# Optimization experiments

Measured on AMD Instinct MI355X. Metric: run time of the kernel, lower is better.

Reference implementation:

```python
import jax, jax.numpy as jnp
import numpy as np

B, C, H, W = 8, 256, 64, 64
CK = 64  # C // k with k=4


def setup_inputs() -> dict:
    key = jax.random.key(0)
    ks = jax.random.split(key, 5)
    s = 1.0 / np.sqrt(C)
    return {
        "x": jax.random.normal(ks[0], (B, C, H, W), dtype=jnp.float32),
        "wq": jax.random.normal(ks[1], (CK, C), dtype=jnp.float32) * s,
        "bq": jnp.zeros((CK,), dtype=jnp.float32),
        "wk": jax.random.normal(ks[2], (CK, C), dtype=jnp.float32) * s,
        "bk": jnp.zeros((CK,), dtype=jnp.float32),
        "wv": jax.random.normal(ks[3], (C, C), dtype=jnp.float32) * s,
        "bv": jnp.zeros((C,), dtype=jnp.float32),
        "wg": jax.random.normal(ks[4], (C, C), dtype=jnp.float32) * s,
        "bg": jnp.zeros((C,), dtype=jnp.float32),
    }


def reference(x, wq, bq, wk, bk, wv, bv, wg, bg):
    b, c, h, w = x.shape
    n = h * w
    xf = x.reshape(b, c, n)  # [B, C, N]
    # 1x1 convs are channel-wise matmuls
    q = jnp.einsum('oc,bcn->bon', wq, xf) + bq[None, :, None]  # [B, Ck, N]
    k = jnp.einsum('oc,bcn->bon', wk, xf) + bk[None, :, None]  # [B, Ck, N]
    v = jnp.einsum('oc,bcn->bon', wv, xf) + bv[None, :, None]  # [B, C, N]
    # energy[b,i,j] = q[b,:,i] . k[b,:,j]
    energy = jnp.einsum('bci,bcj->bij', q, k)  # [B, N, N]
    energy = jax.nn.elu(energy) / n
    out = jnp.einsum('bcn,bnj->bcj', v, energy).reshape(b, c, h, w)
    out = jnp.einsum('oc,bchw->bohw', wg, out) + bg[None, :, None, None]
    return out
```

## Files before the change

### kernel.cpp

```cpp
#include <hip/hip_runtime.h>
#include <math.h>

#define BATCH 8
#define CH    256
#define NPIX  4096
#define CKDIM 64

typedef __attribute__((ext_vector_type(8))) short short8;
typedef __attribute__((ext_vector_type(4))) float f32x4;

#define MFMA16x16(a, b, c) __builtin_amdgcn_mfma_f32_16x16x32_bf16((a), (b), (c), 0, 0, 0)

__device__ __forceinline__ unsigned short f2bf(float f) {
    union { float f; unsigned int u; } v; v.f = f;
    unsigned int u = v.u;
    u += 0x7fffu + ((u >> 16) & 1u);
    return (unsigned short)(u >> 16);
}

__global__ void prep_kernel(const float* __restrict__ wq, const float* __restrict__ bq,
                            const float* __restrict__ wk, const float* __restrict__ bk,
                            const float* __restrict__ wv, const float* __restrict__ bv,
                            const float* __restrict__ wg,
                            unsigned short* __restrict__ W_all, float* __restrict__ bias_all) {
    int o = blockIdx.x;
    int c = threadIdx.x;
    if (o < 64) {
        W_all[o * CH + c] = f2bf(wq[o * CH + c]);
        if (c == 0) bias_all[o] = bq[o];
    } else if (o < 128) {
        int oo = o - 64;
        W_all[o * CH + c] = f2bf(wk[oo * CH + c]);
        if (c == 0) bias_all[o] = bk[oo];
    } else {
        __shared__ float wgr[CH];
        int oo = o - 128;
        wgr[c] = wg[oo * CH + c];
        __syncthreads();
        float a0 = 0.f, a1 = 0.f, a2 = 0.f, a3 = 0.f;
#pragma unroll 4
        for (int m = 0; m < CH; m += 4) {
            a0 += wgr[m + 0] * wv[(m + 0) * CH + c];
            a1 += wgr[m + 1] * wv[(m + 1) * CH + c];
            a2 += wgr[m + 2] * wv[(m + 2) * CH + c];
            a3 += wgr[m + 3] * wv[(m + 3) * CH + c];
        }
        W_all[o * CH + c] = f2bf((a0 + a1) + (a2 + a3));
        if (c == 0) {
            float b = 0.f;
            for (int m = 0; m < CH; ++m) b += wgr[m] * bv[m];
            bias_all[o] = b;
        }
    }
}

__global__ __launch_bounds__(256, 2)
void qkvf_mfma(const float* __restrict__ x,
               const unsigned short* __restrict__ W_all,
               const float* __restrict__ bias_all,
               unsigned short* __restrict__ qk, unsigned short* __restrict__ vp) {
    __shared__ float Tl[64][65];
    __shared__ __align__(16) unsigned short Xl[64][264];

    int n0   = blockIdx.x * 64;
    int b    = blockIdx.y;
    int tid  = threadIdx.x;
    int lane = tid & 63;
    int w    = tid >> 6;
    int col  = lane & 15;
    int quad = lane >> 4;

    for (int c0 = 0; c0 < CH; c0 += 64) {
        if (c0) __syncthreads();
#pragma unroll
        for (int r = 0; r < 4; ++r) {
            int f  = r * 256 + tid;
            int c  = f >> 4;
            int n4 = f & 15;
            float4 v = *(const float4*)(x + ((size_t)b * CH + c0 + c) * NPIX + n0 + n4 * 4);
            Tl[n4 * 4 + 0][c] = v.x;
            Tl[n4 * 4 + 1][c] = v.y;
            Tl[n4 * 4 + 2][c] = v.z;
            Tl[n4 * 4 + 3][c] = v.w;
        }
        __syncthreads();
#pragma unroll
        for (int r = 0; r < 2; ++r) {
            int f    = r * 256 + tid;
            int nrow = f >> 3;
            int c8   = f & 7;
            unsigned int pk[4];
#pragma unroll
            for (int p = 0; p < 4; ++p) {
                unsigned int lo = f2bf(Tl[nrow][c8 * 8 + p * 2 + 0]);
                unsigned int hi = f2bf(Tl[nrow][c8 * 8 + p * 2 + 1]);
                pk[p] = lo | (hi << 16);
            }
            *(uint4*)&Xl[nrow][c0 + c8 * 8] = *(uint4*)pk;
        }
    }
    __syncthreads();

#pragma unroll
    for (int og = 0; og < 6; ++og) {
        int o0 = og * 64;
        const unsigned short* Arow = W_all + (size_t)(o0 + w * 16 + col) * CH + quad * 8;

        f32x4 acc[4];
#pragma unroll
        for (int t = 0; t < 4; ++t) acc[t] = (f32x4){0.f, 0.f, 0.f, 0.f};

#pragma unroll
        for (int kc = 0; kc < 8; ++kc) {
            short8 a = *(const short8*)(Arow + kc * 32);
#pragma unroll
            for (int nt = 0; nt < 4; ++nt) {
                short8 bb = *(const short8*)&Xl[nt * 16 + col][kc * 32 + quad * 8];
                acc[nt] = MFMA16x16(a, bb, acc[nt]);
            }
        }

        float4 bias = *(const float4*)(bias_all + o0 + w * 16 + quad * 4);
        float bs[4] = {bias.x, bias.y, bias.z, bias.w};

        if (og < 2) {
#pragma unroll
            for (int nt = 0; nt < 4; ++nt) {
                int n = n0 + nt * 16 + col;
                unsigned int pk[2];
#pragma unroll
                for (int p = 0; p < 2; ++p) {
                    unsigned int lo = f2bf(acc[nt][p * 2 + 0] + bs[p * 2 + 0]);
                    unsigned int hi = f2bf(acc[nt][p * 2 + 1] + bs[p * 2 + 1]);
                    pk[p] = lo | (hi << 16);
                }
                *(uint2*)(qk + ((size_t)b * NPIX + n) * 128 + o0 + w * 16 + quad * 4) = *(uint2*)pk;
            }
        } else {
#pragma unroll
            for (int nt = 0; nt < 4; ++nt) {
                int n = n0 + nt * 16 + col;
#pragma unroll
                for (int r = 0; r < 4; ++r) {
                    int oo = o0 - 128 + w * 16 + quad * 4 + r;
                    vp[((size_t)b * CH + oo) * NPIX + n] = f2bf(acc[nt][r] + bs[r]);
                }
            }
        }
    }
}

#define LPK 72
__global__ __launch_bounds__(512, 4)
void attn_v11(const unsigned short* __restrict__ qk,
              const unsigned short* __restrict__ vp,
              const float* __restrict__ bg, float* __restrict__ out) {
    __shared__ __align__(16) unsigned short Qt[2][64][LPK];
    __shared__ __align__(16) unsigned short St[2][64][LPK];

    int lin  = blockIdx.y * gridDim.x + blockIdx.x;
    int b    = lin & 7;
    int j0   = (lin >> 3) * 64;
    int tid  = threadIdx.x;
    int lane = tid & 63;
    int w    = tid >> 6;
    int col  = lane & 15;
    int quad = lane >> 4;

    int tjA = w & 3;
    int tiP = (w >> 2) * 2;

    short8 bK[2];
#pragma unroll
    for (int ks = 0; ks < 2; ++ks)
        bK[ks] = *(const short8*)(qk + ((size_t)b * NPIX + j0 + tjA * 16 + col) * 128 + 64 + ks * 32 + quad * 8);

    f32x4 acc[2][4];
#pragma unroll
    for (int ot = 0; ot < 2; ++ot)
#pragma unroll
        for (int tj = 0; tj < 4; ++tj) acc[ot][tj] = (f32x4){0.f, 0.f, 0.f, 0.f};

    int qrow = tid >> 3, q8 = tid & 7;
    const unsigned short* Qsrc = qk + ((size_t)b * NPIX + qrow) * 128 + q8 * 8;
    const unsigned short* Vsrc[2];
#pragma unroll
    for (int ot = 0; ot < 2; ++ot)
        Vsrc[ot] = vp + ((size_t)b * CH + (w * 2 + ot) * 16 + col) * NPIX + quad * 8;

    const float invN = 1.f / (float)NPIX;

    {
        uint4 q0 = *(const uint4*)Qsrc;
        *(uint4*)&Qt[0][qrow][q8 * 8] = q0;
    }
    uint4 qrA = *(const uint4*)(Qsrc + (size_t)64 * 128);
    short8 vb[2][2];
#pragma unroll
    for (int ot = 0; ot < 2; ++ot)
#pragma unroll
        for (int ks = 0; ks < 2; ++ks)
            vb[ot][ks] = *(const short8*)(Vsrc[ot] + ks * 32);

    __syncthreads();

#pragma unroll
    for (int t = 0; t < 2; ++t) {
        int ti = tiP + t;
        short8 a0 = *(const short8*)&Qt[0][ti * 16 + col][quad * 8];
        short8 a1 = *(const short8*)&Qt[0][ti * 16 + col][32 + quad * 8];
        f32x4 s = (f32x4){0.f, 0.f, 0.f, 0.f};
        s = MFMA16x16(a0, bK[0], s);
        s = MFMA16x16(a1, bK[1], s);
        unsigned int pk2[2];
#pragma unroll
        for (int pp = 0; pp < 2; ++pp) {
            float e0 = s[pp * 2 + 0];
            float e1 = s[pp * 2 + 1];
            float g0 = __expf(e0) - 1.f;
            float g1 = __expf(e1) - 1.f;
            e0 = (e0 > 0.f) ? e0 : g0;
            e1 = (e1 > 0.f) ? e1 : g1;
            e0 *= invN;
            e1 *= invN;
            unsigned int rpk;
            asm("v_cvt_pk_bf16_f32 %0, %1, %2" : "=v"(rpk) : "v"(e0), "v"(e1));
            pk2[pp] = rpk;
        }
        *(uint2*)&St[0][tjA * 16 + col][ti * 16 + quad * 4] = *(uint2*)pk2;
    }
    *(uint4*)&Qt[1][qrow][q8 * 8] = qrA;
    qrA = *(const uint4*)(Qsrc + (size_t)(2 * 64) * 128);

    for (int it = 1; it < NPIX / 64; ++it) {
        int pw = it & 1;

        __syncthreads();

        *(uint4*)&Qt[pw ^ 1][qrow][q8 * 8] = qrA;

        {
            size_t iq = (size_t)(((it + 2) * 64) & (NPIX - 1));
            qrA = *(const uint4*)(Qsrc + iq * 128);
        }
        int iv = it * 64;
        short8 vb_n[2][2];
#pragma unroll
        for (int ot = 0; ot < 2; ++ot)
#pragma unroll
            for (int ks = 0; ks < 2; ++ks)
                vb_n[ot][ks] = *(const short8*)(Vsrc[ot] + iv + ks * 32);

#pragma unroll
        for (int ks = 0; ks < 2; ++ks) {
            short8 sb[4];
#pragma unroll
            for (int tj = 0; tj < 4; ++tj)
                sb[tj] = *(const short8*)&St[pw ^ 1][tj * 16 + col][ks * 32 + quad * 8];
            __builtin_amdgcn_s_setprio(1);
#pragma unroll
            for (int ot = 0; ot < 2; ++ot)
#pragma unroll
                for (int tj = 0; tj < 4; ++tj)
                    acc[ot][tj] = MFMA16x16(sb[tj], vb[ot][ks], acc[ot][tj]);
            __builtin_amdgcn_s_setprio(0);
        }

#pragma unroll
        for (int t = 0; t < 2; ++t) {
            int ti = tiP + t;
            short8 a0 = *(const short8*)&Qt[pw][ti * 16 + col][quad * 8];
            short8 a1 = *(const short8*)&Qt[pw][ti * 16 + col][32 + quad * 8];
            f32x4 s = (f32x4){0.f, 0.f, 0.f, 0.f};
            s = MFMA16x16(a0, bK[0], s);
            s = MFMA16x16(a1, bK[1], s);
            unsigned int pk2[2];
#pragma unroll
            for (int pp = 0; pp < 2; ++pp) {
                float e0 = s[pp * 2 + 0];
                float e1 = s[pp * 2 + 1];
                float g0 = __expf(e0) - 1.f;
                float g1 = __expf(e1) - 1.f;
                e0 = (e0 > 0.f) ? e0 : g0;
                e1 = (e1 > 0.f) ? e1 : g1;
                e0 *= invN;
                e1 *= invN;
                unsigned int rpk;
                asm("v_cvt_pk_bf16_f32 %0, %1, %2" : "=v"(rpk) : "v"(e0), "v"(e1));
                pk2[pp] = rpk;
            }
            *(uint2*)&St[pw][tjA * 16 + col][ti * 16 + quad * 4] = *(uint2*)pk2;
        }

#pragma unroll
        for (int ot = 0; ot < 2; ++ot)
#pragma unroll
            for (int ks = 0; ks < 2; ++ks)
                vb[ot][ks] = vb_n[ot][ks];
    }

    __syncthreads();
#pragma unroll
    for (int ks = 0; ks < 2; ++ks) {
        short8 sb[4];
#pragma unroll
        for (int tj = 0; tj < 4; ++tj)
            sb[tj] = *(const short8*)&St[1][tj * 16 + col][ks * 32 + quad * 8];
#pragma unroll
        for (int ot = 0; ot < 2; ++ot)
#pragma unroll
            for (int tj = 0; tj < 4; ++tj)
                acc[ot][tj] = MFMA16x16(sb[tj], vb[ot][ks], acc[ot][tj]);
    }

#pragma unroll
    for (int ot = 0; ot < 2; ++ot) {
        int o = (w * 2 + ot) * 16 + col;
        float bgv = bg[o];
#pragma unroll
        for (int tj = 0; tj < 4; ++tj) {
            int j = j0 + tj * 16 + quad * 4;
            float4 st;
            st.x = acc[ot][tj][0] + bgv;
            st.y = acc[ot][tj][1] + bgv;
            st.z = acc[ot][tj][2] + bgv;
            st.w = acc[ot][tj][3] + bgv;
            *(float4*)&out[((size_t)b * CH + o) * NPIX + j] = st;
        }
    }
}

extern "C" void kernel_launch(void* const* d_in, const int* in_sizes, int n_in,
                              void* d_out, int out_size, void* d_ws, size_t ws_size,
                              hipStream_t stream) {
    const float* x  = (const float*)d_in[0];
    const float* wq = (const float*)d_in[1];
    const float* bq = (const float*)d_in[2];
    const float* wk = (const float*)d_in[3];
    const float* bk = (const float*)d_in[4];
    const float* wv = (const float*)d_in[5];
    const float* bv = (const float*)d_in[6];
    const float* wg = (const float*)d_in[7];
    const float* bg = (const float*)d_in[8];
    float* out = (float*)d_out;

    unsigned short* W_all = (unsigned short*)d_ws;
    float* bias_all = (float*)(W_all + 384 * 256);
    unsigned short* qk = (unsigned short*)(bias_all + 384);
    unsigned short* vp = qk + (size_t)BATCH * NPIX * 128;

    prep_kernel<<<dim3(384), dim3(256), 0, stream>>>(wq, bq, wk, bk, wv, bv, wg, W_all, bias_all);
    qkvf_mfma<<<dim3(NPIX / 64, BATCH), dim3(256), 0, stream>>>(x, W_all, bias_all, qk, vp);
    attn_v11<<<dim3(NPIX / 64, BATCH), dim3(512), 0, stream>>>(qk, vp, bg, out);
}
```

Before: 256.1 us.

## Retile attention PV warps to 4x2 and prestore weights in MFMA fragment order

The attention kernel gives each wave 64 output channels by 32 columns instead of 32 channels by 64 columns. Each wave now reads half as many score fragments from LDS per step but holds twice as many V fragments. The second V k-slice load is deferred until after the first MFMA batch, to spread out register pressure and global latency. Separately, the prep kernel writes the fused weights in MFMA fragment order so the projection kernel gets fully coalesced A loads, and its launch bound is raised to 3 blocks per CU.

```diff
diff --git a/kernel.cpp b/kernel.cpp
--- a/kernel.cpp
+++ b/kernel.cpp
@@ -22,15 +22,17 @@
                             const float* __restrict__ wk, const float* __restrict__ bk,
                             const float* __restrict__ wv, const float* __restrict__ bv,
                             const float* __restrict__ wg,
-                            unsigned short* __restrict__ W_all, float* __restrict__ bias_all) {
+                            unsigned short* __restrict__ W_frag, float* __restrict__ bias_all) {
     int o = blockIdx.x;
     int c = threadIdx.x;
+
+    float val;
     if (o < 64) {
-        W_all[o * CH + c] = f2bf(wq[o * CH + c]);
+        val = wq[o * CH + c];
         if (c == 0) bias_all[o] = bq[o];
     } else if (o < 128) {
         int oo = o - 64;
-        W_all[o * CH + c] = f2bf(wk[oo * CH + c]);
+        val = wk[oo * CH + c];
         if (c == 0) bias_all[o] = bk[oo];
     } else {
         __shared__ float wgr[CH];
@@ -45,18 +47,23 @@
             a2 += wgr[m + 2] * wv[(m + 2) * CH + c];
             a3 += wgr[m + 3] * wv[(m + 3) * CH + c];
         }
-        W_all[o * CH + c] = f2bf((a0 + a1) + (a2 + a3));
+        val = (a0 + a1) + (a2 + a3);
         if (c == 0) {
             float b = 0.f;
             for (int m = 0; m < CH; ++m) b += wgr[m] * bv[m];
             bias_all[o] = b;
         }
     }
-}
-
-__global__ __launch_bounds__(256, 2)
+
+    int og = o >> 6, w = (o >> 4) & 3, col = o & 15;
+    int kc = c >> 5, quad = (c >> 3) & 3, e = c & 7;
+    size_t idx = ((size_t)(((og * 4 + w) * 8 + kc) * 64 + quad * 16 + col)) * 8 + e;
+    W_frag[idx] = f2bf(val);
+}
+
+__global__ __launch_bounds__(256, 3)
 void qkvf_mfma(const float* __restrict__ x,
-               const unsigned short* __restrict__ W_all,
+               const unsigned short* __restrict__ W_frag,
                const float* __restrict__ bias_all,
                unsigned short* __restrict__ qk, unsigned short* __restrict__ vp) {
     __shared__ float Tl[64][65];
@@ -104,7 +111,7 @@
 #pragma unroll
     for (int og = 0; og < 6; ++og) {
         int o0 = og * 64;
-        const unsigned short* Arow = W_all + (size_t)(o0 + w * 16 + col) * CH + quad * 8;
+        const unsigned short* Af = W_frag + ((size_t)(og * 32 + w * 8) << 9);
 
         f32x4 acc[4];
 #pragma unroll
@@ -112,7 +119,7 @@
 
 #pragma unroll
         for (int kc = 0; kc < 8; ++kc) {
-            short8 a = *(const short8*)(Arow + kc * 32);
+            short8 a = *(const short8*)(Af + ((kc << 6) + lane) * 8);
 #pragma unroll
             for (int nt = 0; nt < 4; ++nt) {
                 short8 bb = *(const short8*)&Xl[nt * 16 + col][kc * 32 + quad * 8];
@@ -152,7 +159,7 @@
 
 #define LPK 72
 __global__ __launch_bounds__(512, 4)
-void attn_v11(const unsigned short* __restrict__ qk,
+void attn_v12(const unsigned short* __restrict__ qk,
               const unsigned short* __restrict__ vp,
               const float* __restrict__ bg, float* __restrict__ out) {
     __shared__ __align__(16) unsigned short Qt[2][64][LPK];
@@ -169,24 +176,26 @@
 
     int tjA = w & 3;
     int tiP = (w >> 2) * 2;
+    int og  = w >> 1;
+    int jg  = w & 1;
 
     short8 bK[2];
 #pragma unroll
     for (int ks = 0; ks < 2; ++ks)
         bK[ks] = *(const short8*)(qk + ((size_t)b * NPIX + j0 + tjA * 16 + col) * 128 + 64 + ks * 32 + quad * 8);
 
-    f32x4 acc[2][4];
-#pragma unroll
-    for (int ot = 0; ot < 2; ++ot)
-#pragma unroll
-        for (int tj = 0; tj < 4; ++tj) acc[ot][tj] = (f32x4){0.f, 0.f, 0.f, 0.f};
+    f32x4 acc[4][2];
+#pragma unroll
+    for (int ot = 0; ot < 4; ++ot)
+#pragma unroll
+        for (int tj = 0; tj < 2; ++tj) acc[ot][tj] = (f32x4){0.f, 0.f, 0.f, 0.f};
 
     int qrow = tid >> 3, q8 = tid & 7;
     const unsigned short* Qsrc = qk + ((size_t)b * NPIX + qrow) * 128 + q8 * 8;
-    const unsigned short* Vsrc[2];
-#pragma unroll
-    for (int ot = 0; ot < 2; ++ot)
-        Vsrc[ot] = vp + ((size_t)b * CH + (w * 2 + ot) * 16 + col) * NPIX + quad * 8;
+    const unsigned short* Vsrc[4];
+#pragma unroll
+    for (int ot = 0; ot < 4; ++ot)
+        Vsrc[ot] = vp + ((size_t)b * CH + og * 64 + ot * 16 + col) * NPIX + quad * 8;
 
     const float invN = 1.f / (float)NPIX;
 
@@ -195,12 +204,12 @@
         *(uint4*)&Qt[0][qrow][q8 * 8] = q0;
     }
     uint4 qrA = *(const uint4*)(Qsrc + (size_t)64 * 128);
-    short8 vb[2][2];
-#pragma unroll
-    for (int ot = 0; ot < 2; ++ot)
-#pragma unroll
-        for (int ks = 0; ks < 2; ++ks)
-            vb[ot][ks] = *(const short8*)(Vsrc[ot] + ks * 32);
+    short8 vb0[4], vb1[4], vbn0[4];
+#pragma unroll
+    for (int ot = 0; ot < 4; ++ot) {
+        vb0[ot] = *(const short8*)(Vsrc[ot]);
+        vb1[ot] = *(const short8*)(Vsrc[ot] + 32);
+    }
 
     __syncthreads();
 
@@ -238,33 +247,35 @@
         __syncthreads();
 
         *(uint4*)&Qt[pw ^ 1][qrow][q8 * 8] = qrA;
-
         {
             size_t iq = (size_t)(((it + 2) * 64) & (NPIX - 1));
             qrA = *(const uint4*)(Qsrc + iq * 128);
         }
         int iv = it * 64;
-        short8 vb_n[2][2];
-#pragma unroll
-        for (int ot = 0; ot < 2; ++ot)
-#pragma unroll
-            for (int ks = 0; ks < 2; ++ks)
-                vb_n[ot][ks] = *(const short8*)(Vsrc[ot] + iv + ks * 32);
+#pragma unroll
+        for (int ot = 0; ot < 4; ++ot)
+            vbn0[ot] = *(const short8*)(Vsrc[ot] + iv);
 
 #pragma unroll
         for (int ks = 0; ks < 2; ++ks) {
-            short8 sb[4];
-#pragma unroll
-            for (int tj = 0; tj < 4; ++tj)
-                sb[tj] = *(const short8*)&St[pw ^ 1][tj * 16 + col][ks * 32 + quad * 8];
+            short8 sb[2];
+#pragma unroll
+            for (int tj = 0; tj < 2; ++tj)
+                sb[tj] = *(const short8*)&St[pw ^ 1][jg * 32 + tj * 16 + col][ks * 32 + quad * 8];
             __builtin_amdgcn_s_setprio(1);
 #pragma unroll
-            for (int ot = 0; ot < 2; ++ot)
-#pragma unroll
-                for (int tj = 0; tj < 4; ++tj)
-                    acc[ot][tj] = MFMA16x16(sb[tj], vb[ot][ks], acc[ot][tj]);
+            for (int ot = 0; ot < 4; ++ot) {
+                short8 v = (ks == 0) ? vb0[ot] : vb1[ot];
+#pragma unroll
+                for (int tj = 0; tj < 2; ++tj)
+                    acc[ot][tj] = MFMA16x16(sb[tj], v, acc[ot][tj]);
+            }
             __builtin_amdgcn_s_setprio(0);
         }
+
+#pragma unroll
+        for (int ot = 0; ot < 4; ++ot)
+            vb1[ot] = *(const short8*)(Vsrc[ot] + iv + 32);
 
 #pragma unroll
         for (int t = 0; t < 2; ++t) {
@@ -293,33 +304,33 @@
         }
 
 #pragma unroll
-        for (int ot = 0; ot < 2; ++ot)
-#pragma unroll
-            for (int ks = 0; ks < 2; ++ks)
-                vb[ot][ks] = vb_n[ot][ks];
+        for (int ot = 0; ot < 4; ++ot)
+            vb0[ot] = vbn0[ot];
     }
 
     __syncthreads();
 #pragma unroll
     for (int ks = 0; ks < 2; ++ks) {
-        short8 sb[4];
-#pragma unroll
-        for (int tj = 0; tj < 4; ++tj)
-            sb[tj] = *(const short8*)&St[1][tj * 16 + col][ks * 32 + quad * 8];
-#pragma unroll
-        for (int ot = 0; ot < 2; ++ot)
-#pragma unroll
-            for (int tj = 0; tj < 4; ++tj)
-                acc[ot][tj] = MFMA16x16(sb[tj], vb[ot][ks], acc[ot][tj]);
-    }
-
-#pragma unroll
-    for (int ot = 0; ot < 2; ++ot) {
-        int o = (w * 2 + ot) * 16 + col;
+        short8 sb[2];
+#pragma unroll
+        for (int tj = 0; tj < 2; ++tj)
+            sb[tj] = *(const short8*)&St[1][jg * 32 + tj * 16 + col][ks * 32 + quad * 8];
+#pragma unroll
+        for (int ot = 0; ot < 4; ++ot) {
+            short8 v = (ks == 0) ? vb0[ot] : vb1[ot];
+#pragma unroll
+            for (int tj = 0; tj < 2; ++tj)
+                acc[ot][tj] = MFMA16x16(sb[tj], v, acc[ot][tj]);
+        }
+    }
+
+#pragma unroll
+    for (int ot = 0; ot < 4; ++ot) {
+        int o = og * 64 + ot * 16 + col;
         float bgv = bg[o];
 #pragma unroll
-        for (int tj = 0; tj < 4; ++tj) {
-            int j = j0 + tj * 16 + quad * 4;
+        for (int tj = 0; tj < 2; ++tj) {
+            int j = j0 + jg * 32 + tj * 16 + quad * 4;
             float4 st;
             st.x = acc[ot][tj][0] + bgv;
             st.y = acc[ot][tj][1] + bgv;
@@ -344,12 +355,12 @@
     const float* bg = (const float*)d_in[8];
     float* out = (float*)d_out;
 
-    unsigned short* W_all = (unsigned short*)d_ws;
-    float* bias_all = (float*)(W_all + 384 * 256);
+    unsigned short* W_frag = (unsigned short*)d_ws;
+    float* bias_all = (float*)(W_frag + 384 * 256);
     unsigned short* qk = (unsigned short*)(bias_all + 384);
     unsigned short* vp = qk + (size_t)BATCH * NPIX * 128;
 
-    prep_kernel<<<dim3(384), dim3(256), 0, stream>>>(wq, bq, wk, bk, wv, bv, wg, W_all, bias_all);
-    qkvf_mfma<<<dim3(NPIX / 64, BATCH), dim3(256), 0, stream>>>(x, W_all, bias_all, qk, vp);
-    attn_v11<<<dim3(NPIX / 64, BATCH), dim3(512), 0, stream>>>(qk, vp, bg, out);
-}
+    prep_kernel<<<dim3(384), dim3(256), 0, stream>>>(wq, bq, wk, bk, wv, bv, wg, W_frag, bias_all);
+    qkvf_mfma<<<dim3(NPIX / 64, BATCH), dim3(256), 0, stream>>>(x, W_frag, bias_all, qk, vp);
+    attn_v12<<<dim3(NPIX / 64, BATCH), dim3(512), 0, stream>>>(qk, vp, bg, out);
+}
```

Result: slower. 357.1 us (+39.4%).
